# Kernel optimization log

Measured on AMD Instinct MI355X. Metric: run time of the kernel, lower is better.

The kernel has to match this reference:

```python
import jax, jax.numpy as jnp
import numpy as np

EPS = 1e-9
NEG_BIG = -(2.0**32) + 1.0


def dice(x, alpha):
    # BN with center=False, scale=False at inference: moving_mean=0, moving_var=1
    x_norm = x * (1.0 / np.sqrt(1.0 + EPS)).astype(np.float32)
    p = jax.nn.sigmoid(x_norm)
    return alpha * (1.0 - p) * x + p * x


def setup_inputs() -> dict:
    key = jax.random.key(0)
    ks = jax.random.split(key, 12)
    B, T, D = 4096, 200, 128
    U = 128  # gru units == hidden_dim

    def glorot(k, shape):
        fan_in = shape[0]
        return (jax.random.normal(k, shape, dtype=jnp.float32) / np.sqrt(fan_in)).astype(jnp.float32)

    return {
        "interest_seq": jax.random.normal(ks[0], (B, T, D), dtype=jnp.float32),
        "target_emb": jax.random.normal(ks[1], (B, D), dtype=jnp.float32),
        "seq_length": jax.random.randint(ks[2], (B, 1), 0, T, dtype=jnp.int32),
        "W_att1": glorot(ks[3], (4 * D, 64)),
        "alpha1": jnp.zeros((64,), jnp.float32),
        "W_att2": glorot(ks[4], (64, 16)),
        "alpha2": jnp.zeros((16,), jnp.float32),
        "W_att3": glorot(ks[5], (16, 1)),
        "W_u": glorot(ks[6], (D + U, U)),
        "W_r": glorot(ks[7], (D + U, U)),
        "W_c": glorot(ks[8], (D + U, U)),
    }


def reference(interest_seq, target_emb, seq_length, W_att1, alpha1, W_att2, alpha2, W_att3, W_u, W_r, W_c):
    B, T, D = interest_seq.shape
    U = W_u.shape[1]

    # ---- Attention scores (return_score=True, sigmoid, no weight norm) ----
    q = jnp.broadcast_to(target_emb[:, None, :], (B, T, D))  # [B,T,D]
    k = interest_seq
    att_in = jnp.concatenate([q, k, q - k, q * k], axis=-1)  # [B,T,4D]
    h1 = dice(jnp.einsum('btf,fh->bth', att_in, W_att1), alpha1)
    h2 = dice(jnp.einsum('bth,hg->btg', h1, W_att2), alpha2)
    score = jnp.einsum('btg,go->bto', h2, W_att3)  # [B,T,1]

    valid = jnp.arange(T)[None, :] < seq_length  # [B,T] bool
    vmask = valid.astype(jnp.float32)[:, :, None]
    score = score * vmask + (1.0 - vmask) * NEG_BIG
    att = jax.nn.sigmoid(score)[:, :, 0]  # [B,T]

    # ---- AUGRU scan (return final hidden state) ----
    def step(h, xs):
        x_t, a_t, m_t = xs  # [B,D], [B], [B] bool
        gi = jnp.concatenate([x_t, h], axis=-1)  # [B, D+U]
        u = jax.nn.sigmoid(gi @ W_u)
        r = jax.nn.sigmoid(gi @ W_r)
        c = jnp.tanh(jnp.concatenate([x_t, r * h], axis=-1) @ W_c)
        u_t = u * a_t[:, None]
        h_new = (1.0 - u_t) * h + u_t * c
        h = jnp.where(m_t[:, None], h_new, h)
        return h, None

    xs = (jnp.swapaxes(interest_seq, 0, 1),  # [T,B,D]
          att.T,                              # [T,B]
          valid.T)                            # [T,B]
    h0 = jnp.zeros((B, U), dtype=interest_seq.dtype)
    h_final, _ = jax.lax.scan(step, h0, xs)
    return h_final
```

## Files before the change

### kernel.cpp

```cpp
#include <hip/hip_runtime.h>
#include <math.h>

typedef __bf16 bf16;
typedef __bf16 bf16x8 __attribute__((ext_vector_type(8)));
typedef float  f32x4  __attribute__((ext_vector_type(4)));

#define MFMA16(a,b,c) __builtin_amdgcn_mfma_f32_16x16x32_bf16((a),(b),(c),0,0,0)

#define B_SZ 4096
#define T_SZ 200
#define D_SZ 128
#define U_SZ 128
#define ACHUNK 4
#define AROWS 16
#define ATTB 8

__device__ __forceinline__ float frcp_(float x) { return __builtin_amdgcn_rcpf(x); }
__device__ __forceinline__ float fsig(float x)  { return frcp_(1.0f + __expf(-x)); }
__device__ __forceinline__ float ftanh_(float x){ return 1.0f - 2.0f * frcp_(1.0f + __expf(2.0f * x)); }
__device__ __forceinline__ float dicef(float x, float alpha) {
    float p = fsig(x);
    return alpha * (1.0f - p) * x + p * x;
}

__global__ __launch_bounds__(256) void prep_kernel(
    const float* __restrict__ Q,
    const float* __restrict__ W1,
    const float* __restrict__ W2,
    float* __restrict__ BIAS,
    bf16*  __restrict__ W1P,
    bf16*  __restrict__ W2T)
{
    const int tid = threadIdx.x;
    if (blockIdx.x == 256) {
        #pragma unroll 4
        for (int it = 0; it < 64; ++it) {
            int idx = it * 256 + tid;
            int k = idx >> 6;
            int n = idx & 63;
            float v;
            if (k < 128) v = W1[(128 + k) * 64 + n] - W1[(256 + k) * 64 + n];
            else         v = W1[(384 + (k - 128)) * 64 + n];
            W1P[n * 256 + k] = (bf16)v;
        }
        #pragma unroll
        for (int it = 0; it < 4; ++it) {
            int idx = it * 256 + tid; int k = idx >> 4; int n = idx & 15;
            W2T[n * 64 + k] = (bf16)W2[k * 16 + n];
        }
        return;
    }
    const int b0   = blockIdx.x * 16;
    const int lane = tid & 63;
    const int w    = tid >> 6;
    const int quad = lane >> 4;
    const int l15  = lane & 15;

    bf16x8 a[4];
    #pragma unroll
    for (int kk = 0; kk < 4; ++kk) {
        const float* p = Q + (long)(b0 + l15) * D_SZ + kk * 32 + quad * 8;
        float4 x0 = ((const float4*)p)[0];
        float4 x1 = ((const float4*)p)[1];
        float xv[8] = {x0.x, x0.y, x0.z, x0.w, x1.x, x1.y, x1.z, x1.w};
        #pragma unroll
        for (int j = 0; j < 8; ++j) a[kk][j] = (bf16)xv[j];
    }
    const int n = w * 16 + l15;
    f32x4 acc = {};
    #pragma unroll
    for (int kk = 0; kk < 4; ++kk) {
        bf16x8 bf;
        #pragma unroll
        for (int j = 0; j < 8; ++j) {
            int k = kk * 32 + quad * 8 + j;
            bf[j] = (bf16)(W1[k * 64 + n] + W1[(256 + k) * 64 + n]);
        }
        acc = MFMA16(a[kk], bf, acc);
    }
    #pragma unroll
    for (int i = 0; i < 4; ++i)
        BIAS[(long)(b0 + quad * 4 + i) * 64 + n] = acc[i];
}

__global__ __launch_bounds__(256) void attn_kernel(
    const float* __restrict__ X,
    const float* __restrict__ Q,
    const int*   __restrict__ LEN,
    const float* __restrict__ A1,
    const float* __restrict__ A2,
    const float* __restrict__ W3,
    const float* __restrict__ BIAS,
    const bf16*  __restrict__ W1P,
    const bf16*  __restrict__ W2T,
    float* __restrict__ ATT)
{
    __shared__ bf16  H1s[64][72];
    __shared__ float qf[ATTB][128];
    __shared__ float bias_s[ATTB][64];
    __shared__ float al1[64];
    __shared__ float al2[16];
    __shared__ float w3s[16];
    __shared__ int   lens[ATTB];

    const int tid  = threadIdx.x;
    const int lane = tid & 63;
    const int w    = tid >> 6;
    const int quad = lane >> 4;
    const int l15  = lane & 15;
    const long b0  = (long)blockIdx.x * ATTB;

    for (int i = tid; i < ATTB * 128; i += 256) qf[i >> 7][i & 127] = Q[b0 * 128 + i];
    for (int i = tid; i < ATTB * 64;  i += 256) bias_s[i >> 6][i & 63] = BIAS[b0 * 64 + i];
    if (tid < 64) al1[tid] = A1[tid];
    if (tid < 16) { al2[tid] = A2[tid]; w3s[tid] = W3[tid]; }
    if (tid < ATTB) lens[tid] = LEN[b0 + tid];

    bf16x8 b1[4][8];
    #pragma unroll
    for (int nt = 0; nt < 4; ++nt)
        #pragma unroll
        for (int kk = 0; kk < 8; ++kk)
            b1[nt][kk] = *(const bf16x8*)(W1P + (nt * 16 + l15) * 256 + kk * 32 + quad * 8);
    bf16x8 b2[2];
    #pragma unroll
    for (int kk = 0; kk < 2; ++kk)
        b2[kk] = *(const bf16x8*)(W2T + l15 * 64 + kk * 32 + quad * 8);
    __syncthreads();

    const int NT = 13 * ATTB;
    float4 fb[8];
    auto issue = [&](int g) {
        int bi = g / 13, mt = g - bi * 13;
        int row = mt * 16 + l15;
        int rc  = row < T_SZ ? row : (T_SZ - 1);
        const float* xp = X + ((b0 + bi) * T_SZ + rc) * D_SZ;
        #pragma unroll
        for (int kc = 0; kc < 4; ++kc) {
            const float* p = xp + kc * 32 + quad * 8;
            fb[kc * 2]     = ((const float4*)p)[0];
            fb[kc * 2 + 1] = ((const float4*)p)[1];
        }
    };
    auto convert = [&](int g, bf16x8* axd, bf16x8* aqd) {
        int bi = g / 13;
        #pragma unroll
        for (int kc = 0; kc < 4; ++kc) {
            float4 xa = fb[kc * 2], xb = fb[kc * 2 + 1];
            float xv[8] = {xa.x, xa.y, xa.z, xa.w, xb.x, xb.y, xb.z, xb.w};
            const float* qp = &qf[bi][kc * 32 + quad * 8];
            #pragma unroll
            for (int j = 0; j < 8; ++j) {
                axd[kc][j] = (bf16)xv[j];
                aqd[kc][j] = (bf16)(xv[j] * qp[j]);
            }
        }
    };

    bf16x8 axc[4], aqc[4];
    issue(w);
    convert(w, axc, aqc);

    for (int g = w; g < NT; g += 4) {
        const int gn = g + 4;
        if (gn < NT) issue(gn);

        f32x4 acc[4] = {};
        #pragma unroll
        for (int kc = 0; kc < 4; ++kc)
            #pragma unroll
            for (int nt = 0; nt < 4; ++nt) {
                acc[nt] = MFMA16(axc[kc], b1[nt][kc],     acc[nt]);
                acc[nt] = MFMA16(aqc[kc], b1[nt][kc + 4], acc[nt]);
            }

        const int bi = g / 13, mt = g - bi * 13;
        const int m0 = mt * 16;
        #pragma unroll
        for (int nt = 0; nt < 4; ++nt) {
            int n = nt * 16 + l15;
            float bia = bias_s[bi][n]; float al = al1[n];
            #pragma unroll
            for (int i = 0; i < 4; ++i) {
                float v = acc[nt][i] + bia;
                H1s[w * 16 + quad * 4 + i][n] = (bf16)dicef(v, al);
            }
        }
        f32x4 acc2 = {};
        #pragma unroll
        for (int kk = 0; kk < 2; ++kk) {
            bf16x8 a2 = *(const bf16x8*)&H1s[w * 16 + l15][kk * 32 + quad * 8];
            acc2 = MFMA16(a2, b2[kk], acc2);
        }
        {
            float al = al2[l15]; float w3 = w3s[l15];
            float s[4];
            #pragma unroll
            for (int i = 0; i < 4; ++i) s[i] = dicef(acc2[i], al) * w3;
            #pragma unroll
            for (int i = 0; i < 4; ++i) {
                s[i] += __shfl_xor(s[i], 1, 64);
                s[i] += __shfl_xor(s[i], 2, 64);
                s[i] += __shfl_xor(s[i], 4, 64);
                s[i] += __shfl_xor(s[i], 8, 64);
            }
            if (l15 == 0) {
                int len = lens[bi];
                #pragma unroll
                for (int i = 0; i < 4; ++i) {
                    int t = m0 + quad * 4 + i;
                    if (t < T_SZ)
                        ATT[(b0 + bi) * T_SZ + t] = (t < len) ? fsig(s[i]) : 0.0f;
                }
            }
        }
        if (gn < NT) convert(gn, axc, aqc);
    }
}

__global__ __launch_bounds__(512) void augru_kernel(
    const float* __restrict__ X,
    const float* __restrict__ ATT,
    const float* __restrict__ WU,
    const float* __restrict__ WR,
    const float* __restrict__ WC,
    float* __restrict__ OUT)
{
    __shared__ bf16  Xs[2][ACHUNK][16][136];
    __shared__ float As[2][ACHUNK][16];
    __shared__ bf16  Hb[16][136];
    __shared__ bf16  RHb[16][136];

    const int tid  = threadIdx.x;
    const int lane = tid & 63;
    const int w    = tid >> 6;
    const int quad = lane >> 4;
    const int l15  = lane & 15;
    const int b0   = blockIdx.x * AROWS;
    const int n    = w * 16 + l15;

    for (int i = tid; i < 16 * 136; i += 512) { ((bf16*)Hb)[i] = (bf16)0.f; ((bf16*)RHb)[i] = (bf16)0.f; }

    bf16x8 Wf[3][2][4];
    {
        const float* Wg[3] = {WU, WR, WC};
        #pragma unroll
        for (int g = 0; g < 3; ++g)
            #pragma unroll
            for (int p = 0; p < 2; ++p)
                #pragma unroll
                for (int kk = 0; kk < 4; ++kk) {
                    #pragma unroll
                    for (int i = 0; i < 8; ++i) {
                        int k = p * 128 + kk * 32 + quad * 8 + i;
                        Wf[g][p][kk][i] = (bf16)Wg[g][k * 128 + n];
                    }
                }
    }

    float h[4] = {0.f, 0.f, 0.f, 0.f};

    float4 pf[4];
    float  pa = 0.f;
    auto issue_loads = [&](int c) {
        #pragma unroll
        for (int it = 0; it < 4; ++it) {
            int gidx = it * 512 + tid;
            int c4 = gidx & 31;
            int pair = gidx >> 5;
            int r = pair & 15;
            int s = pair >> 4;
            pf[it] = *(const float4*)(X + ((long)(b0 + r) * T_SZ + (c * ACHUNK + s)) * D_SZ + c4 * 4);
        }
        if (tid < ACHUNK * 16) {
            int r = tid & 15; int s = tid >> 4;
            pa = ATT[(long)(b0 + r) * T_SZ + c * ACHUNK + s];
        }
    };
    auto commit = [&](int buf) {
        #pragma unroll
        for (int it = 0; it < 4; ++it) {
            int gidx = it * 512 + tid;
            int c4 = gidx & 31;
            int pair = gidx >> 5;
            int r = pair & 15;
            int s = pair >> 4;
            bf16* dst = &Xs[buf][s][r][c4 * 4];
            float4 v = pf[it];
            dst[0] = (bf16)v.x; dst[1] = (bf16)v.y; dst[2] = (bf16)v.z; dst[3] = (bf16)v.w;
        }
        if (tid < ACHUNK * 16) { int r = tid & 15; int s = tid >> 4; As[buf][s][r] = pa; }
    };

    issue_loads(0);
    commit(0);
    __syncthreads();

    const int NCH = T_SZ / ACHUNK;
    for (int c = 0; c < NCH; ++c) {
        const int buf = c & 1;
        if (c + 1 < NCH) issue_loads(c + 1);

        #pragma unroll
        for (int s = 0; s < ACHUNK; ++s) {
            bf16x8 ax[4], ah[4];
            #pragma unroll
            for (int kk = 0; kk < 4; ++kk) {
                ax[kk] = *(const bf16x8*)&Xs[buf][s][l15][kk * 32 + quad * 8];
                ah[kk] = *(const bf16x8*)&Hb[l15][kk * 32 + quad * 8];
            }
            f32x4 pr = {};
            #pragma unroll
            for (int kk = 0; kk < 4; ++kk) pr = MFMA16(ax[kk], Wf[1][0][kk], pr);
            #pragma unroll
            for (int kk = 0; kk < 4; ++kk) pr = MFMA16(ah[kk], Wf[1][1][kk], pr);
            #pragma unroll
            for (int i = 0; i < 4; ++i) {
                int row = quad * 4 + i;
                float rr = fsig(pr[i]);
                RHb[row][n] = (bf16)(rr * h[i]);
            }
            f32x4 pu = {}, pc = {};
            #pragma unroll
            for (int kk = 0; kk < 4; ++kk) {
                pu = MFMA16(ax[kk], Wf[0][0][kk], pu);
                pu = MFMA16(ah[kk], Wf[0][1][kk], pu);
                pc = MFMA16(ax[kk], Wf[2][0][kk], pc);
            }
            __syncthreads();
            bf16x8 ar[4];
            #pragma unroll
            for (int kk = 0; kk < 4; ++kk)
                ar[kk] = *(const bf16x8*)&RHb[l15][kk * 32 + quad * 8];
            #pragma unroll
            for (int kk = 0; kk < 4; ++kk) pc = MFMA16(ar[kk], Wf[2][1][kk], pc);
            #pragma unroll
            for (int i = 0; i < 4; ++i) {
                int row = quad * 4 + i;
                float a  = As[buf][s][row];
                float u  = fsig(pu[i]);
                float cg = ftanh_(pc[i]);
                float ut = u * a;
                float hn = (1.f - ut) * h[i] + ut * cg;
                h[i] = hn;
                Hb[row][n] = (bf16)hn;
            }
            __syncthreads();
        }
        if (c + 1 < NCH) commit(buf ^ 1);
        __syncthreads();
    }

    #pragma unroll
    for (int i = 0; i < 4; ++i)
        OUT[(long)(b0 + quad * 4 + i) * U_SZ + n] = h[i];
}

extern "C" void kernel_launch(void* const* d_in, const int* in_sizes, int n_in,
                              void* d_out, int out_size, void* d_ws, size_t ws_size,
                              hipStream_t stream) {
    const float* X   = (const float*)d_in[0];
    const float* Q   = (const float*)d_in[1];
    const int*   LEN = (const int*)d_in[2];
    const float* W1  = (const float*)d_in[3];
    const float* A1  = (const float*)d_in[4];
    const float* W2  = (const float*)d_in[5];
    const float* A2  = (const float*)d_in[6];
    const float* W3  = (const float*)d_in[7];
    const float* WU  = (const float*)d_in[8];
    const float* WR  = (const float*)d_in[9];
    const float* WC  = (const float*)d_in[10];
    float* OUT = (float*)d_out;

    float* ATT  = (float*)d_ws;
    float* BIAS = ATT + (size_t)B_SZ * T_SZ;
    bf16*  W1P  = (bf16*)(BIAS + (size_t)B_SZ * 64);
    bf16*  W2T  = W1P + 64 * 256;

    prep_kernel<<<257, 256, 0, stream>>>(Q, W1, W2, BIAS, W1P, W2T);
    attn_kernel<<<B_SZ / ATTB, 256, 0, stream>>>(X, Q, LEN, A1, A2, W3, BIAS, W1P, W2T, ATT);
    augru_kernel<<<B_SZ / AROWS, 512, 0, stream>>>(X, ATT, WU, WR, WC, OUT);
}
```

Measured before the change: 813.7 us.

## Software-pipeline input projections and spread LDS commits across AUGRU steps

Moves the x-dependent MFMA products for the next timestep ahead of the current step's finishing elementwise work, so they overlap the recurrent critical path. The staged bf16 commit of the next chunk is split across the four inner steps, which removes one barrier per chunk. __syncthreads is replaced by a raw lgkmcnt wait plus s_barrier. This raises register pressure from the carried accumulators. The hand-written barrier also relies on LDS-only waits being sufficient for correctness.

```diff
diff --git a/kernel.cpp b/kernel.cpp
--- a/kernel.cpp
+++ b/kernel.cpp
@@ -21,6 +21,9 @@
 __device__ __forceinline__ float dicef(float x, float alpha) {
     float p = fsig(x);
     return alpha * (1.0f - p) * x + p * x;
+}
+__device__ __forceinline__ void bar_lgkm() {
+    asm volatile("s_waitcnt lgkmcnt(0)\n\ts_barrier" ::: "memory");
 }
 
 __global__ __launch_bounds__(256) void prep_kernel(
@@ -277,24 +280,39 @@
             pa = ATT[(long)(b0 + r) * T_SZ + c * ACHUNK + s];
         }
     };
-    auto commit = [&](int buf) {
-        #pragma unroll
-        for (int it = 0; it < 4; ++it) {
-            int gidx = it * 512 + tid;
-            int c4 = gidx & 31;
-            int pair = gidx >> 5;
-            int r = pair & 15;
-            int s = pair >> 4;
-            bf16* dst = &Xs[buf][s][r][c4 * 4];
-            float4 v = pf[it];
-            dst[0] = (bf16)v.x; dst[1] = (bf16)v.y; dst[2] = (bf16)v.z; dst[3] = (bf16)v.w;
-        }
-        if (tid < ACHUNK * 16) { int r = tid & 15; int s = tid >> 4; As[buf][s][r] = pa; }
+    auto commit_part = [&](int buf, int it) {
+        int gidx = it * 512 + tid;
+        int c4 = gidx & 31;
+        int pair = gidx >> 5;
+        int r = pair & 15;
+        int s = pair >> 4;
+        bf16* dst = &Xs[buf][s][r][c4 * 4];
+        float4 v = pf[it];
+        dst[0] = (bf16)v.x; dst[1] = (bf16)v.y; dst[2] = (bf16)v.z; dst[3] = (bf16)v.w;
+        if (it == 0 && tid < ACHUNK * 16) {
+            int r2 = tid & 15; int s2 = tid >> 4;
+            As[buf][s2][r2] = pa;
+        }
+    };
+    auto xparts = [&](int buf, int s, f32x4& pr_, f32x4& pu_, f32x4& pc_) {
+        f32x4 r0 = {}, u0 = {}, c0 = {};
+        #pragma unroll
+        for (int kk = 0; kk < 4; ++kk) {
+            bf16x8 ax = *(const bf16x8*)&Xs[buf][s][l15][kk * 32 + quad * 8];
+            r0 = MFMA16(ax, Wf[1][0][kk], r0);
+            u0 = MFMA16(ax, Wf[0][0][kk], u0);
+            c0 = MFMA16(ax, Wf[2][0][kk], c0);
+        }
+        pr_ = r0; pu_ = u0; pc_ = c0;
     };
 
     issue_loads(0);
-    commit(0);
-    __syncthreads();
+    #pragma unroll
+    for (int it = 0; it < 4; ++it) commit_part(0, it);
+    bar_lgkm();
+
+    f32x4 pr, pu, pc;
+    xparts(0, 0, pr, pu, pc);
 
     const int NCH = T_SZ / ACHUNK;
     for (int c = 0; c < NCH; ++c) {
@@ -303,52 +321,46 @@
 
         #pragma unroll
         for (int s = 0; s < ACHUNK; ++s) {
-            bf16x8 ax[4], ah[4];
+            bf16x8 ah[4];
+            #pragma unroll
+            for (int kk = 0; kk < 4; ++kk)
+                ah[kk] = *(const bf16x8*)&Hb[l15][kk * 32 + quad * 8];
             #pragma unroll
             for (int kk = 0; kk < 4; ++kk) {
-                ax[kk] = *(const bf16x8*)&Xs[buf][s][l15][kk * 32 + quad * 8];
-                ah[kk] = *(const bf16x8*)&Hb[l15][kk * 32 + quad * 8];
-            }
-            f32x4 pr = {};
-            #pragma unroll
-            for (int kk = 0; kk < 4; ++kk) pr = MFMA16(ax[kk], Wf[1][0][kk], pr);
-            #pragma unroll
-            for (int kk = 0; kk < 4; ++kk) pr = MFMA16(ah[kk], Wf[1][1][kk], pr);
+                pr = MFMA16(ah[kk], Wf[1][1][kk], pr);
+                pu = MFMA16(ah[kk], Wf[0][1][kk], pu);
+            }
+            float uu[4];
             #pragma unroll
             for (int i = 0; i < 4; ++i) {
-                int row = quad * 4 + i;
                 float rr = fsig(pr[i]);
-                RHb[row][n] = (bf16)(rr * h[i]);
-            }
-            f32x4 pu = {}, pc = {};
-            #pragma unroll
-            for (int kk = 0; kk < 4; ++kk) {
-                pu = MFMA16(ax[kk], Wf[0][0][kk], pu);
-                pu = MFMA16(ah[kk], Wf[0][1][kk], pu);
-                pc = MFMA16(ax[kk], Wf[2][0][kk], pc);
-            }
-            __syncthreads();
+                RHb[quad * 4 + i][n] = (bf16)(rr * h[i]);
+                uu[i] = fsig(pu[i]);
+            }
+            bar_lgkm();
             bf16x8 ar[4];
             #pragma unroll
             for (int kk = 0; kk < 4; ++kk)
                 ar[kk] = *(const bf16x8*)&RHb[l15][kk * 32 + quad * 8];
             #pragma unroll
-            for (int kk = 0; kk < 4; ++kk) pc = MFMA16(ar[kk], Wf[2][1][kk], pc);
+            for (int kk = 0; kk < 4; ++kk)
+                pc = MFMA16(ar[kk], Wf[2][1][kk], pc);
+            f32x4 prN, puN, pcN;
+            if (s + 1 < ACHUNK) xparts(buf, s + 1, prN, puN, pcN);
             #pragma unroll
             for (int i = 0; i < 4; ++i) {
-                int row = quad * 4 + i;
-                float a  = As[buf][s][row];
-                float u  = fsig(pu[i]);
+                float a  = As[buf][s][quad * 4 + i];
                 float cg = ftanh_(pc[i]);
-                float ut = u * a;
+                float ut = uu[i] * a;
                 float hn = (1.f - ut) * h[i] + ut * cg;
                 h[i] = hn;
-                Hb[row][n] = (bf16)hn;
-            }
-            __syncthreads();
-        }
-        if (c + 1 < NCH) commit(buf ^ 1);
-        __syncthreads();
+                Hb[quad * 4 + i][n] = (bf16)hn;
+            }
+            if (c + 1 < NCH) commit_part(buf ^ 1, s);
+            bar_lgkm();
+            if (s + 1 < ACHUNK) { pr = prN; pu = puN; pc = pcN; }
+        }
+        if (c + 1 < NCH) xparts(buf ^ 1, 0, pr, pu, pc);
     }
 
     #pragma unroll
```

Result: slower. 833.1 us (+2.4%).
